# Kernel optimization log

Measured on AMD Instinct MI355X. Metric: run time of the kernel, lower is better.

## Reference

```python
import jax, jax.numpy as jnp
import numpy as np
import math

B, L, D, H = 4, 1024, 1024, 16
HD = D // H  # head dim = 64


def setup_inputs() -> dict:
    key = jax.random.key(0)
    ks = jax.random.split(key, 8)
    s = 1.0 / math.sqrt(D)
    return {
        "Q": jax.random.normal(ks[0], (B, L, D), jnp.float32),
        "K": jax.random.normal(ks[1], (B, L, D), jnp.float32),
        "V": jax.random.normal(ks[2], (B, L, D), jnp.float32),
        "valid_lens": jax.random.randint(ks[3], (B * H * L,), 0, L, jnp.int32),
        "Wq": jax.random.normal(ks[4], (D, D), jnp.float32) * s,
        "Wk": jax.random.normal(ks[5], (D, D), jnp.float32) * s,
        "Wv": jax.random.normal(ks[6], (D, D), jnp.float32) * s,
        "Wo": jax.random.normal(ks[7], (D, D), jnp.float32) * s,
    }


def _split_heads(X):
    # [B, L, D] -> [B*H, L, HD]
    return X.reshape(B, L, H, HD).transpose(0, 2, 1, 3).reshape(B * H, L, HD)


def reference(Q, K, V, valid_lens, Wq, Wk, Wv, Wo):
    q = _split_heads(Q @ Wq.T)
    k = _split_heads(K @ Wk.T)
    v = _split_heads(V @ Wv.T)
    # scaled dot-product scores: [B*H, Lq, Lk]
    scores = jnp.einsum("bqd,bkd->bqk", q, k) / math.sqrt(HD)
    # original flattens scores to [B*H*Lq, Lk] and masks with a
    # [len(valid_lens), Lq] mask (Lq == Lk here) of -1e6, then softmax
    mask = jnp.arange(L)[None, :] < valid_lens[:, None]  # [B*H*L, L]
    flat = jnp.where(mask, scores.reshape(-1, L), jnp.float32(-1e6))
    attn = jax.nn.softmax(flat, axis=-1).reshape(B * H, L, L)
    out = jnp.einsum("bqk,bkd->bqd", attn, v)  # dropout p=0 is identity
    # merge heads: [B*H, L, HD] -> [B, L, D]
    out = out.reshape(B, H, L, HD).transpose(0, 2, 1, 3).reshape(B, L, D)
    return out @ Wo.T
```

## Files before the change

### kernel.cpp

```cpp
#include <hip/hip_runtime.h>
#include <hip/hip_bf16.h>

typedef short v8s __attribute__((ext_vector_type(8)));
typedef unsigned short v8u __attribute__((ext_vector_type(8)));
typedef float v4f __attribute__((ext_vector_type(4)));
typedef unsigned short u16;

#define LL 1024
#define DD 1024

static __device__ __forceinline__ u16 f2b(float x) {
  __hip_bfloat16 h = __float2bfloat16(x);
  return __builtin_bit_cast(u16, h);
}
static __device__ __forceinline__ float b2f(u16 u) {
  unsigned int x = ((unsigned int)u) << 16;
  return __builtin_bit_cast(float, x);
}

static __device__ __forceinline__ void gload_lds16(const u16* g, u16* l) {
  __builtin_amdgcn_global_load_lds((const __attribute__((address_space(1))) void*)g,
                                   (__attribute__((address_space(3))) void*)l, 16, 0, 0);
}

__global__ __launch_bounds__(256) void cvt3(const float* __restrict__ p0,
                                            const float* __restrict__ p1,
                                            const float* __restrict__ p2,
                                            u16* __restrict__ out, int n8, long ostride) {
  const float* src = blockIdx.y == 0 ? p0 : (blockIdx.y == 1 ? p1 : p2);
  u16* dst = out + (long)blockIdx.y * ostride;
  int i = blockIdx.x * 256 + threadIdx.x;
  if (i >= n8) return;
  const float4* p = (const float4*)src + (long)i * 2;
  float4 a = p[0], b = p[1];
  v8u r;
  r[0] = f2b(a.x); r[1] = f2b(a.y); r[2] = f2b(a.z); r[3] = f2b(a.w);
  r[4] = f2b(b.x); r[5] = f2b(b.y); r[6] = f2b(b.z); r[7] = f2b(b.w);
  *((v8u*)dst + i) = r;
}

__global__ __launch_bounds__(256) void sortperm(const int* __restrict__ valid,
                                                u16* __restrict__ perm) {
  __shared__ int hist[1024];
  __shared__ int wsum[4];
  const int bh = blockIdx.x;
  const int tid = threadIdx.x;
  const int* v = valid + bh * 1024;
  for (int i = tid; i < 1024; i += 256) hist[i] = 0;
  __syncthreads();
  for (int i = tid; i < 1024; i += 256) {
    int k = v[i];
    k = (k == 0) ? 1023 : (k - 1);
    atomicAdd(&hist[k], 1);
  }
  __syncthreads();
  const int base = tid * 4;
  int h0 = hist[base], h1 = hist[base + 1], h2 = hist[base + 2], h3 = hist[base + 3];
  int local = h0 + h1 + h2 + h3;
  const int lane = tid & 63, w = tid >> 6;
  int scan = local;
#pragma unroll
  for (int d = 1; d < 64; d <<= 1) {
    int t = __shfl_up(scan, d);
    if (lane >= d) scan += t;
  }
  if (lane == 63) wsum[w] = scan;
  __syncthreads();
  int woff = 0;
  for (int i = 0; i < w; ++i) woff += wsum[i];
  int excl = woff + scan - local;
  hist[base] = excl;
  hist[base + 1] = excl + h0;
  hist[base + 2] = excl + h0 + h1;
  hist[base + 3] = excl + h0 + h1 + h2;
  __syncthreads();
  for (int i = tid; i < 1024; i += 256) {
    int k = v[i];
    k = (k == 0) ? 1023 : (k - 1);
    int pos = atomicAdd(&hist[k], 1);
    perm[bh * 1024 + pos] = (u16)i;
  }
}

template <typename OUTT>
__global__ __launch_bounds__(256) void gemm_bt(const u16* __restrict__ A,
                                               const u16* __restrict__ Bw,
                                               OUTT* __restrict__ C,
                                               long za, long zb, long zc) {
  __shared__ u16 As[128 * 64];
  __shared__ u16 Bs[128 * 64];
  A += (long)blockIdx.z * za;
  Bw += (long)blockIdx.z * zb;
  C += (long)blockIdx.z * zc;
  const int tid = threadIdx.x;
  const int lane = tid & 63;
  const int l15 = lane & 15, lg = lane >> 4;
  const int wid = tid >> 6;
  const int wm = wid >> 1, wn = wid & 1;
  const long mbase = (long)blockIdx.y * 128;
  const long nbase = (long)blockIdx.x * 128;

  const u16* ap = A + (mbase + (tid >> 3)) * 1024 + (tid & 7) * 8;
  const u16* bp = Bw + (nbase + (tid >> 3)) * 1024 + (tid & 7) * 8;

  v4f acc[4][4] = {};

  for (int kt = 0; kt < 16; ++kt) {
    __syncthreads();
#pragma unroll
    for (int j = 0; j < 4; ++j) {
      gload_lds16(ap + kt * 64 + j * 32 * 1024, &As[(tid + 256 * j) * 8]);
      gload_lds16(bp + kt * 64 + j * 32 * 1024, &Bs[(tid + 256 * j) * 8]);
    }
    __syncthreads();
#pragma unroll
    for (int kk = 0; kk < 2; ++kk) {
      v8s a[4], b[4];
#pragma unroll
      for (int i = 0; i < 4; ++i)
        a[i] = *(const v8s*)&As[(wm * 64 + i * 16 + l15) * 64 + kk * 32 + lg * 8];
#pragma unroll
      for (int i = 0; i < 4; ++i)
        b[i] = *(const v8s*)&Bs[(wn * 64 + i * 16 + l15) * 64 + kk * 32 + lg * 8];
#pragma unroll
      for (int mi = 0; mi < 4; ++mi)
#pragma unroll
        for (int nj = 0; nj < 4; ++nj)
          acc[mi][nj] = __builtin_amdgcn_mfma_f32_16x16x32_bf16(a[mi], b[nj], acc[mi][nj], 0, 0, 0);
    }
  }
#pragma unroll
  for (int mi = 0; mi < 4; ++mi) {
#pragma unroll
    for (int r = 0; r < 4; ++r) {
      long row = mbase + wm * 64 + mi * 16 + lg * 4 + r;
#pragma unroll
      for (int nj = 0; nj < 4; ++nj) {
        long col = nbase + wn * 64 + nj * 16 + l15;
        if constexpr (__is_same(OUTT, float))
          C[row * 1024 + col] = acc[mi][nj][r];
        else
          C[row * 1024 + col] = f2b(acc[mi][nj][r]);
      }
    }
  }
}

__global__ __launch_bounds__(256) void attn_kern(const u16* __restrict__ qb,
                                                 const u16* __restrict__ kb,
                                                 const u16* __restrict__ vb,
                                                 const int* __restrict__ valid,
                                                 const u16* __restrict__ perm,
                                                 u16* __restrict__ partO,
                                                 float* __restrict__ partM,
                                                 float* __restrict__ partL) {
  __shared__ u16 Ks[64 * 72];
  __shared__ u16 Vt[64 * 72];
  __shared__ u16 Ps[4][16 * 72];

  const int tid = threadIdx.x;
  const int lane = tid & 63;
  const int wid = tid >> 6;
  const int l15 = lane & 15, lg = lane >> 4;
  const int bh = blockIdx.y;
  const int b = bh >> 4, h = bh & 15;
  const long headoff = ((long)b * LL) * DD + h * 64;
  const int xx = blockIdx.x;
  const int gq = 15 - (xx >> 1);
  const int ch = xx & 1;
  const u16* pblk = perm + bh * 1024 + gq * 64;

  const int lastv = valid[bh * LL + pblk[63]];
  const int ntiles = ((lastv == 0 ? LL : lastv) + 63) >> 6;
  const int kt0 = ch * 8;
  const int kt1 = min(ntiles, kt0 + 8);
  if (kt0 >= kt1) return;
  const int slot = (bh * 16 + gq) * 2 + ch;

  const u16* pp = pblk + wid * 16;

  const int qrowA = pp[l15];
  v8s qf[2];
#pragma unroll
  for (int ks = 0; ks < 2; ++ks)
    qf[ks] = *(const v8s*)(qb + headoff + (long)qrowA * DD + ks * 32 + lg * 8);

  int vraw[4];
#pragma unroll
  for (int r = 0; r < 4; ++r) vraw[r] = valid[bh * LL + pp[lg * 4 + r]];

  float mrow[4], lrow[4];
  v4f oacc[4] = {};
#pragma unroll
  for (int r = 0; r < 4; ++r) { mrow[r] = -1e30f; lrow[r] = 0.0f; }

  const int kk = tid & 63;
  const int qtr = tid >> 6;
  const long stagebase = headoff + (long)kk * DD + qtr * 16;

  v8s rk0 = *(const v8s*)(kb + stagebase + (long)kt0 * 64 * DD);
  v8s rk1 = *(const v8s*)(kb + stagebase + (long)kt0 * 64 * DD + 8);
  v8s rv0 = *(const v8s*)(vb + stagebase + (long)kt0 * 64 * DD);
  v8s rv1 = *(const v8s*)(vb + stagebase + (long)kt0 * 64 * DD + 8);

  for (int kt = kt0; kt < kt1; ++kt) {
    __builtin_amdgcn_sched_barrier(0);
    __builtin_amdgcn_s_barrier();
    __builtin_amdgcn_sched_barrier(0);

    *(v8s*)&Ks[kk * 72 + qtr * 16] = rk0;
    *(v8s*)&Ks[kk * 72 + qtr * 16 + 8] = rk1;
    {
      v8u u0 = __builtin_bit_cast(v8u, rv0);
      v8u u1 = __builtin_bit_cast(v8u, rv1);
#pragma unroll
      for (int j = 0; j < 8; ++j) Vt[(qtr * 16 + j) * 72 + kk] = u0[j];
#pragma unroll
      for (int j = 0; j < 8; ++j) Vt[(qtr * 16 + 8 + j) * 72 + kk] = u1[j];
    }
    if (kt + 1 < kt1) {
      const long noff = stagebase + (long)(kt + 1) * 64 * DD;
      rk0 = *(const v8s*)(kb + noff);
      rk1 = *(const v8s*)(kb + noff + 8);
      rv0 = *(const v8s*)(vb + noff);
      rv1 = *(const v8s*)(vb + noff + 8);
    }
    asm volatile("s_waitcnt lgkmcnt(0)" ::: "memory");
    __builtin_amdgcn_sched_barrier(0);
    __builtin_amdgcn_s_barrier();
    __builtin_amdgcn_sched_barrier(0);

    v4f s[4];
    __builtin_amdgcn_s_setprio(1);
#pragma unroll
    for (int t = 0; t < 4; ++t) {
      v4f z = {};
#pragma unroll
      for (int ks = 0; ks < 2; ++ks) {
        v8s kf = *(const v8s*)&Ks[(t * 16 + l15) * 72 + ks * 32 + lg * 8];
        z = __builtin_amdgcn_mfma_f32_16x16x32_bf16(qf[ks], kf, z, 0, 0, 0);
      }
      s[t] = z;
    }
    __builtin_amdgcn_s_setprio(0);

    const float SC = 0.18033688f;
    const int colbase = kt * 64 + l15;
#pragma unroll
    for (int t = 0; t < 4; ++t)
#pragma unroll
      for (int r = 0; r < 4; ++r) {
        float val = s[t][r] * SC;
        s[t][r] = (colbase + t * 16 < vraw[r]) ? val : -1e6f;
      }

    float pm[4];
#pragma unroll
    for (int r = 0; r < 4; ++r)
      pm[r] = fmaxf(fmaxf(s[0][r], s[1][r]), fmaxf(s[2][r], s[3][r]));
#pragma unroll
    for (int d = 1; d < 16; d <<= 1)
#pragma unroll
      for (int r = 0; r < 4; ++r) pm[r] = fmaxf(pm[r], __shfl_xor(pm[r], d));

    bool sk = true;
#pragma unroll
    for (int r = 0; r < 4; ++r) sk = sk && (pm[r] <= mrow[r] + 11.0f);
    if (!__all(sk)) {
#pragma unroll
      for (int r = 0; r < 4; ++r) {
        float mn = fmaxf(mrow[r], pm[r]);
        float sc = __builtin_amdgcn_exp2f(mrow[r] - mn);
        mrow[r] = mn;
        lrow[r] *= sc;
#pragma unroll
        for (int t = 0; t < 4; ++t) oacc[t][r] *= sc;
      }
    }
    float rs[4] = {0.f, 0.f, 0.f, 0.f};
#pragma unroll
    for (int t = 0; t < 4; ++t)
#pragma unroll
      for (int r = 0; r < 4; ++r) {
        float p = __builtin_amdgcn_exp2f(s[t][r] - mrow[r]);
        s[t][r] = p;
        rs[r] += p;
      }
#pragma unroll
    for (int d = 1; d < 16; d <<= 1)
#pragma unroll
      for (int r = 0; r < 4; ++r) rs[r] += __shfl_xor(rs[r], d);
#pragma unroll
    for (int r = 0; r < 4; ++r) lrow[r] += rs[r];

#pragma unroll
    for (int t = 0; t < 4; ++t)
#pragma unroll
      for (int r = 0; r < 4; ++r)
        Ps[wid][(lg * 4 + r) * 72 + t * 16 + l15] = f2b(s[t][r]);

    asm volatile("s_waitcnt lgkmcnt(0)" ::: "memory");
    __builtin_amdgcn_sched_barrier(0);

    __builtin_amdgcn_s_setprio(1);
#pragma unroll
    for (int ks = 0; ks < 2; ++ks) {
      v8s pa = *(const v8s*)&Ps[wid][l15 * 72 + ks * 32 + lg * 8];
#pragma unroll
      for (int t = 0; t < 4; ++t) {
        v8s vf = *(const v8s*)&Vt[(t * 16 + l15) * 72 + ks * 32 + lg * 8];
        oacc[t] = __builtin_amdgcn_mfma_f32_16x16x32_bf16(pa, vf, oacc[t], 0, 0, 0);
      }
    }
    __builtin_amdgcn_s_setprio(0);
  }

  u16* po = partO + (long)slot * 4096;
  float* pmv = partM + slot * 64;
  float* plv = partL + slot * 64;
#pragma unroll
  for (int r = 0; r < 4; ++r) {
    int p = wid * 16 + lg * 4 + r;
    pmv[p] = mrow[r];
    plv[p] = lrow[r];
#pragma unroll
    for (int t = 0; t < 4; ++t)
      po[p * 64 + t * 16 + l15] = f2b(oacc[t][r]);
  }
}

__global__ __launch_bounds__(256) void merge_kern(const int* __restrict__ valid,
                                                  const u16* __restrict__ perm,
                                                  const u16* __restrict__ partO,
                                                  const float* __restrict__ partM,
                                                  const float* __restrict__ partL,
                                                  u16* __restrict__ ob) {
  const int g = blockIdx.x, bh = blockIdx.y;
  const int b = bh >> 4, h = bh & 15;
  const u16* pblk = perm + bh * 1024 + g * 64;
  const int lastv = valid[bh * LL + pblk[63]];
  const int ntiles = ((lastv == 0 ? LL : lastv) + 63) >> 6;
  const bool has1 = ntiles > 8;
  const int p = threadIdx.x >> 2;
  const int q4 = (threadIdx.x & 3) * 16;
  const int s0 = (bh * 16 + g) * 2;

  float m0 = partM[s0 * 64 + p], l0 = partL[s0 * 64 + p];
  float w0 = 1.0f, w1 = 0.0f, L = l0;
  if (has1) {
    float m1 = partM[(s0 + 1) * 64 + p], l1 = partL[(s0 + 1) * 64 + p];
    float M = fmaxf(m0, m1);
    w0 = __builtin_amdgcn_exp2f(m0 - M);
    w1 = __builtin_amdgcn_exp2f(m1 - M);
    L = l0 * w0 + l1 * w1;
  }
  const float inv = 1.0f / L;

  const u16* po0 = partO + (long)s0 * 4096 + p * 64 + q4;
  float acc[16];
  {
    v8u x0 = *(const v8u*)po0;
    v8u x1 = *(const v8u*)(po0 + 8);
#pragma unroll
    for (int j = 0; j < 8; ++j) acc[j] = b2f(x0[j]) * w0;
#pragma unroll
    for (int j = 0; j < 8; ++j) acc[8 + j] = b2f(x1[j]) * w0;
  }
  if (has1) {
    const u16* po1 = po0 + 4096;
    v8u y0 = *(const v8u*)po1;
    v8u y1 = *(const v8u*)(po1 + 8);
#pragma unroll
    for (int j = 0; j < 8; ++j) acc[j] += b2f(y0[j]) * w1;
#pragma unroll
    for (int j = 0; j < 8; ++j) acc[8 + j] += b2f(y1[j]) * w1;
  }
  const int orow = pblk[p];
  u16* dst = ob + ((long)b * LL + orow) * DD + h * 64 + q4;
#pragma unroll
  for (int j = 0; j < 16; ++j) dst[j] = f2b(acc[j] * inv);
}

extern "C" void kernel_launch(void* const* d_in, const int* in_sizes, int n_in,
                              void* d_out, int out_size, void* d_ws, size_t ws_size,
                              hipStream_t stream) {
  const float* Q = (const float*)d_in[0];
  const float* K = (const float*)d_in[1];
  const float* V = (const float*)d_in[2];
  const int* valid = (const int*)d_in[3];
  const float* Wq = (const float*)d_in[4];
  const float* Wk = (const float*)d_in[5];
  const float* Wv = (const float*)d_in[6];
  const float* Wo = (const float*)d_in[7];
  float* out = (float*)d_out;

  u16* ws = (u16*)d_ws;
  const long MK = 4096L * 1024;
  const long NK = 1024L * 1024;
  u16* qkvb = ws;
  u16* wqkv = qkvb + 3 * MK;
  u16* wo = wqkv + 3 * NK;
  u16* proj = wo + NK;
  u16* ob = proj + 3 * MK;
  u16* perm = wqkv;
  u16* partO = qkvb;
  float* partM = (float*)(qkvb + 2048L * 4096);
  float* partL = partM + 2048L * 64;

  cvt3<<<dim3(2048, 3), 256, 0, stream>>>(Q, K, V, qkvb, (int)(MK / 8), MK);
  cvt3<<<dim3(512, 3), 256, 0, stream>>>(Wq, Wk, Wv, wqkv, (int)(NK / 8), NK);
  cvt3<<<dim3(512, 1), 256, 0, stream>>>(Wo, Wo, Wo, wo, (int)(NK / 8), 0);

  gemm_bt<u16><<<dim3(8, 32, 3), 256, 0, stream>>>(qkvb, wqkv, proj, MK, NK, MK);
  sortperm<<<64, 256, 0, stream>>>(valid, perm);
  attn_kern<<<dim3(32, 64), 256, 0, stream>>>(proj, proj + MK, proj + 2 * MK, valid,
                                              perm, partO, partM, partL);
  merge_kern<<<dim3(16, 64), 256, 0, stream>>>(valid, perm, partO, partM, partL, ob);
  gemm_bt<float><<<dim3(8, 32, 1), 256, 0, stream>>>(ob, wo, out, 0, 0, 0);
}
```

Measured before the change: 157.2 us.

## Load K fragments directly from global and double-buffer V tile in LDS

Drops the K staging through LDS: each wave now loads its K MFMA fragments straight from global memory into registers. V is written into a double-buffered LDS tile, so only one block barrier per iteration is needed, placed after the softmax and before the PV MFMAs. The goal is less LDS traffic and fewer barriers. In exchange, each wave issues redundant uncoalesced global K loads with exposed latency, since they are not prefetched a tile ahead.

```diff
diff --git a/kernel.cpp b/kernel.cpp
--- a/kernel.cpp
+++ b/kernel.cpp
@@ -154,8 +154,7 @@
                                                  u16* __restrict__ partO,
                                                  float* __restrict__ partM,
                                                  float* __restrict__ partL) {
-  __shared__ u16 Ks[64 * 72];
-  __shared__ u16 Vt[64 * 72];
+  __shared__ u16 Vt[2][64 * 72];
   __shared__ u16 Ps[4][16 * 72];
 
   const int tid = threadIdx.x;
@@ -197,38 +196,35 @@
   const int kk = tid & 63;
   const int qtr = tid >> 6;
   const long stagebase = headoff + (long)kk * DD + qtr * 16;
-
-  v8s rk0 = *(const v8s*)(kb + stagebase + (long)kt0 * 64 * DD);
-  v8s rk1 = *(const v8s*)(kb + stagebase + (long)kt0 * 64 * DD + 8);
+  const u16* kbh = kb + headoff;
+
   v8s rv0 = *(const v8s*)(vb + stagebase + (long)kt0 * 64 * DD);
   v8s rv1 = *(const v8s*)(vb + stagebase + (long)kt0 * 64 * DD + 8);
 
   for (int kt = kt0; kt < kt1; ++kt) {
-    __builtin_amdgcn_sched_barrier(0);
-    __builtin_amdgcn_s_barrier();
-    __builtin_amdgcn_sched_barrier(0);
-
-    *(v8s*)&Ks[kk * 72 + qtr * 16] = rk0;
-    *(v8s*)&Ks[kk * 72 + qtr * 16 + 8] = rk1;
+    const int cur = kt & 1;
     {
       v8u u0 = __builtin_bit_cast(v8u, rv0);
       v8u u1 = __builtin_bit_cast(v8u, rv1);
 #pragma unroll
-      for (int j = 0; j < 8; ++j) Vt[(qtr * 16 + j) * 72 + kk] = u0[j];
-#pragma unroll
-      for (int j = 0; j < 8; ++j) Vt[(qtr * 16 + 8 + j) * 72 + kk] = u1[j];
-    }
+      for (int j = 0; j < 8; ++j) Vt[cur][(qtr * 16 + j) * 72 + kk] = u0[j];
+#pragma unroll
+      for (int j = 0; j < 8; ++j) Vt[cur][(qtr * 16 + 8 + j) * 72 + kk] = u1[j];
+    }
+
+    const u16* ktb = kbh + (long)(kt * 64) * DD;
+    v8s kf[4][2];
+#pragma unroll
+    for (int t = 0; t < 4; ++t)
+#pragma unroll
+      for (int ks = 0; ks < 2; ++ks)
+        kf[t][ks] = *(const v8s*)(ktb + (long)(t * 16 + l15) * DD + ks * 32 + lg * 8);
+
     if (kt + 1 < kt1) {
       const long noff = stagebase + (long)(kt + 1) * 64 * DD;
-      rk0 = *(const v8s*)(kb + noff);
-      rk1 = *(const v8s*)(kb + noff + 8);
       rv0 = *(const v8s*)(vb + noff);
       rv1 = *(const v8s*)(vb + noff + 8);
     }
-    asm volatile("s_waitcnt lgkmcnt(0)" ::: "memory");
-    __builtin_amdgcn_sched_barrier(0);
-    __builtin_amdgcn_s_barrier();
-    __builtin_amdgcn_sched_barrier(0);
 
     v4f s[4];
     __builtin_amdgcn_s_setprio(1);
@@ -236,10 +232,8 @@
     for (int t = 0; t < 4; ++t) {
       v4f z = {};
 #pragma unroll
-      for (int ks = 0; ks < 2; ++ks) {
-        v8s kf = *(const v8s*)&Ks[(t * 16 + l15) * 72 + ks * 32 + lg * 8];
-        z = __builtin_amdgcn_mfma_f32_16x16x32_bf16(qf[ks], kf, z, 0, 0, 0);
-      }
+      for (int ks = 0; ks < 2; ++ks)
+        z = __builtin_amdgcn_mfma_f32_16x16x32_bf16(qf[ks], kf[t][ks], z, 0, 0, 0);
       s[t] = z;
     }
     __builtin_amdgcn_s_setprio(0);
@@ -293,6 +287,11 @@
 #pragma unroll
     for (int r = 0; r < 4; ++r) lrow[r] += rs[r];
 
+    asm volatile("s_waitcnt lgkmcnt(0)" ::: "memory");
+    __builtin_amdgcn_sched_barrier(0);
+    __builtin_amdgcn_s_barrier();
+    __builtin_amdgcn_sched_barrier(0);
+
 #pragma unroll
     for (int t = 0; t < 4; ++t)
 #pragma unroll
@@ -308,7 +307,7 @@
       v8s pa = *(const v8s*)&Ps[wid][l15 * 72 + ks * 32 + lg * 8];
 #pragma unroll
       for (int t = 0; t < 4; ++t) {
-        v8s vf = *(const v8s*)&Vt[(t * 16 + l15) * 72 + ks * 32 + lg * 8];
+        v8s vf = *(const v8s*)&Vt[cur][(t * 16 + l15) * 72 + ks * 32 + lg * 8];
         oacc[t] = __builtin_amdgcn_mfma_f32_16x16x32_bf16(pa, vf, oacc[t], 0, 0, 0);
       }
     }
```

New measurement: 179.0 us. 13.9% more time.
